# Performance work log

Hardware: AMD Instinct MI355X
Metric: run time of the kernel (lower is better)

## Reference

```python
import jax, jax.numpy as jnp
import numpy as np

NEG_SLOPE = 0.2  # PyG GATConv LeakyReLU slope
EPS = 1e-16


def _add_self_loops(edge_index, num_nodes):
    loops = jnp.arange(num_nodes, dtype=edge_index.dtype)
    return jnp.concatenate([edge_index, jnp.stack([loops, loops])], axis=1)


def _gat_conv(x, src, dst, W, a_src, a_dst, bias, heads, out_ch, concat, num_nodes):
    # x: [N, F_in]; W: [F_in, heads*out_ch]
    h = (x @ W).reshape(num_nodes, heads, out_ch)            # [N, H, C]
    alpha_s = jnp.einsum('nhc,hc->nh', h, a_src)              # [N, H]
    alpha_d = jnp.einsum('nhc,hc->nh', h, a_dst)              # [N, H]
    e = jax.nn.leaky_relu(alpha_s[src] + alpha_d[dst], NEG_SLOPE)  # [E, H]
    # segment softmax over incoming edges of each destination node
    e_max = jax.ops.segment_max(e, dst, num_segments=num_nodes)
    e = jnp.exp(e - e_max[dst])
    denom = jax.ops.segment_sum(e, dst, num_segments=num_nodes)
    alpha = e / (denom[dst] + EPS)                             # [E, H]
    msg = h[src] * alpha[:, :, None]                           # [E, H, C]
    out = jax.ops.segment_sum(msg, dst, num_segments=num_nodes)  # [N, H, C]
    out = out.reshape(num_nodes, heads * out_ch) if concat else out.mean(axis=1)
    return out + bias


def setup_inputs() -> dict:
    key = jax.random.key(0)
    ks = jax.random.split(key, 10)
    N, F_in, H, C1, classes, E = 50000, 128, 8, 16, 40, 1600000
    return {
        'x': jax.random.normal(ks[0], (N, F_in), jnp.float32),
        'edge_index': jax.random.randint(ks[1], (2, E), 0, N, jnp.int64),
        'W1': jax.random.normal(ks[2], (F_in, H * C1), jnp.float32) * (1.0 / np.sqrt(F_in)),
        'a_src1': jax.random.normal(ks[3], (H, C1), jnp.float32) * 0.1,
        'a_dst1': jax.random.normal(ks[4], (H, C1), jnp.float32) * 0.1,
        'b1': jax.random.normal(ks[5], (H * C1,), jnp.float32) * 0.01,
        'W2': jax.random.normal(ks[6], (H * C1, classes), jnp.float32) * (1.0 / np.sqrt(H * C1)),
        'a_src2': jax.random.normal(ks[7], (1, classes), jnp.float32) * 0.1,
        'a_dst2': jax.random.normal(ks[8], (1, classes), jnp.float32) * 0.1,
        'b2': jax.random.normal(ks[9], (classes,), jnp.float32) * 0.01,
    }


def reference(x, edge_index, W1, a_src1, a_dst1, b1, W2, a_src2, a_dst2, b2):
    N = x.shape[0]
    ei = _add_self_loops(edge_index, N)
    src, dst = ei[0], ei[1]
    h = _gat_conv(x, src, dst, W1, a_src1, a_dst1, b1, heads=8, out_ch=16, concat=True, num_nodes=N)
    h = jax.nn.elu(h)
    out = _gat_conv(h, src, dst, W2, a_src2, a_dst2, b2, heads=1, out_ch=40, concat=False, num_nodes=N)
    return out
```

## Files before the change

### kernel.cpp

```cpp
#include <hip/hip_runtime.h>
#include <hip/hip_bf16.h>
#include <hip/hip_fp16.h>

#define NEG_SLOPE 0.2f
#define EPSV 1e-16f
#define CAP 96
#define CHUNK 4096
#define BCAP 9216

static __device__ __forceinline__ float lrelu(float v) {
    return v > 0.0f ? v : NEG_SLOPE * v;
}
static __device__ __forceinline__ float eluf(float v) {
    return v > 0.0f ? v : (__expf(v) - 1.0f);
}

__global__ __launch_bounds__(256) void k_fused1(
    const float* __restrict__ x, const float* __restrict__ W,
    const float* __restrict__ a_src, const float* __restrict__ a_dst,
    const int* __restrict__ ei, int E, int N, int AB,
    __half* __restrict__ h, float* __restrict__ as, float* __restrict__ ad,
    int* __restrict__ gcur, unsigned* __restrict__ bbuf) {
    __shared__ float wl[64 * 128];
    __shared__ float xl[32 * 64];
    const int tid = threadIdx.x;

    if ((int)blockIdx.x < AB) {
        int* cnt = (int*)wl;
        int* base = ((int*)wl) + 256;
        int e0 = blockIdx.x * CHUNK;
        int dreg[16], sreg[16];
#pragma unroll
        for (int jj = 0; jj < 16; ++jj) {
            int e = e0 + tid + jj * 256;
            dreg[jj] = (e < E) ? ei[E + e] : -1;
            sreg[jj] = (e < E) ? ei[e] : 0;
        }
        cnt[tid] = 0;
        __syncthreads();
#pragma unroll
        for (int jj = 0; jj < 16; ++jj)
            if (dreg[jj] >= 0) atomicAdd(&cnt[dreg[jj] >> 8], 1);
        __syncthreads();
        {
            int c = cnt[tid];
            base[tid] = c ? atomicAdd(&gcur[tid], c) : 0;
            cnt[tid] = 0;
        }
        __syncthreads();
#pragma unroll
        for (int jj = 0; jj < 16; ++jj) {
            int d = dreg[jj];
            if (d >= 0) {
                int b = d >> 8;
                int k = atomicAdd(&cnt[b], 1);
                bbuf[(size_t)b * BCAP + base[b] + k] =
                    (unsigned)sreg[jj] | ((unsigned)(d & 255) << 16);
            }
        }
        return;
    }

    const int row0 = (blockIdx.x - AB) * 32;
    const int c0 = (tid & 31) * 4;
    const int r0 = (tid >> 5) * 4;
    float acc[4][4];
#pragma unroll
    for (int r = 0; r < 4; ++r)
#pragma unroll
        for (int c = 0; c < 4; ++c) acc[r][c] = 0.0f;

    for (int kt = 0; kt < 128; kt += 64) {
        __syncthreads();
#pragma unroll
        for (int i = tid * 4; i < 64 * 128; i += 1024)
            *(float4*)&wl[i] = *(const float4*)&W[kt * 128 + i];
#pragma unroll
        for (int i = tid * 4; i < 32 * 64; i += 1024) {
            int r = i >> 6, c = i & 63;
            int gr = row0 + r;
            float4 v = make_float4(0.f, 0.f, 0.f, 0.f);
            if (gr < N) v = *(const float4*)&x[(size_t)gr * 128 + kt + c];
            *(float4*)&xl[i] = v;
        }
        __syncthreads();
#pragma unroll 8
        for (int k = 0; k < 64; ++k) {
            float4 w4 = *(const float4*)&wl[k * 128 + c0];
#pragma unroll
            for (int r = 0; r < 4; ++r) {
                float xv = xl[(r0 + r) * 64 + k];
                acc[r][0] = fmaf(xv, w4.x, acc[r][0]);
                acc[r][1] = fmaf(xv, w4.y, acc[r][1]);
                acc[r][2] = fmaf(xv, w4.z, acc[r][2]);
                acc[r][3] = fmaf(xv, w4.w, acc[r][3]);
            }
        }
    }
#pragma unroll
    for (int r = 0; r < 4; ++r) {
        int gr = row0 + r0 + r;
        if (gr < N) {
            __half2 q0 = __floats2half2_rn(acc[r][0], acc[r][1]);
            __half2 q1 = __floats2half2_rn(acc[r][2], acc[r][3]);
            uint2 st;
            st.x = *(unsigned*)&q0;
            st.y = *(unsigned*)&q1;
            *(uint2*)&h[(size_t)gr * 128 + c0] = st;
        }
    }
    float4 asv = *(const float4*)&a_src[c0];
    float4 adv = *(const float4*)&a_dst[c0];
#pragma unroll
    for (int r = 0; r < 4; ++r) {
        float sp = acc[r][0] * asv.x + acc[r][1] * asv.y + acc[r][2] * asv.z +
                   acc[r][3] * asv.w;
        float dp = acc[r][0] * adv.x + acc[r][1] * adv.y + acc[r][2] * adv.z +
                   acc[r][3] * adv.w;
        sp += __shfl_xor(sp, 1, 64);
        sp += __shfl_xor(sp, 2, 64);
        dp += __shfl_xor(dp, 1, 64);
        dp += __shfl_xor(dp, 2, 64);
        int gr = row0 + r0 + r;
        if ((tid & 3) == 0 && gr < N) {
            int hd = (tid & 31) >> 2;
            as[(size_t)gr * 8 + hd] = sp;
            ad[(size_t)gr * 8 + hd] = dp;
        }
    }
}

__global__ __launch_bounds__(256) void k_csr2(const unsigned* __restrict__ bbuf,
                                              const int* __restrict__ gcnt, int N,
                                              int* __restrict__ deg,
                                              unsigned short* __restrict__ srcs) {
    __shared__ unsigned short rows[256 * CAP];
    __shared__ int cnt[256];
    const int b = blockIdx.x, tid = threadIdx.x;
    cnt[tid] = 0;
    __syncthreads();
    int nb = gcnt[b];
    const unsigned* bp = &bbuf[(size_t)b * BCAP];
    for (int i = tid; i < nb; i += 256) {
        unsigned u = bp[i];
        int dlo = u >> 16;
        int k = atomicAdd(&cnt[dlo], 1);
        rows[dlo * CAP + k] = (unsigned short)(u & 0xFFFFu);
    }
    __syncthreads();
    int n = (b << 8) + tid;
    if (n < N) deg[n] = cnt[tid];
    int maxn = N - (b << 8);
    if (maxn > 256) maxn = 256;
    if (maxn < 0) maxn = 0;
    const unsigned* r32 = (const unsigned*)rows;
    unsigned* g32 = (unsigned*)srcs;
    size_t gbase = (size_t)(b << 8) * (CAP / 2);
    int lim = maxn * (CAP / 2);
    for (int i = tid; i < lim; i += 256) g32[gbase + i] = r32[i];
}

__global__ __launch_bounds__(256) void k_agg1(const int* __restrict__ deg,
                                              const unsigned short* __restrict__ srcs,
                                              const float* __restrict__ as1,
                                              const float* __restrict__ ad1,
                                              const __half* __restrict__ h1,
                                              const float* __restrict__ b1,
                                              __half* __restrict__ hout, int N) {
    int wid = threadIdx.x >> 6, lane = threadIdx.x & 63;
    int n = blockIdx.x * 4 + wid;
    if (n >= N) return;
    size_t st = (size_t)n * CAP;
    int tot = deg[n] + 1;
    int q = lane >> 4;
    int j = lane & 15;
    int es = lane >> 3;
    int hq = lane & 7;
    float adv = ad1[(size_t)n * 8 + hq];
    float l = 0.f;
    float acc[8];
#pragma unroll
    for (int k = 0; k < 8; ++k) acc[k] = 0.f;

    for (int base = 0; base < tot; base += 64) {
        int rem = tot - base;
        if (rem > 64) rem = 64;
        int gi = base + lane;
        int sreg = (gi < tot - 1) ? (int)srcs[st + gi] : n;
        for (int bb = 0; bb < rem; bb += 8) {
            int sp = __shfl(sreg, bb + es, 64);
            float pv = __expf(lrelu(as1[(size_t)sp * 8 + hq] + adv));
            if (bb + es >= rem) pv = 0.f;
            l += pv;
#pragma unroll
            for (int t = 0; t < 8; t += 4) {
                int er = t + q;
                int s = __shfl(sreg, bb + er, 64);
                float p = __shfl(pv, (er << 3) | (j >> 1), 64);
                uint4 u = *(const uint4*)&h1[(size_t)s * 128 + (j << 3)];
                const __half2* hp2 = (const __half2*)&u;
#pragma unroll
                for (int k2 = 0; k2 < 4; ++k2) {
                    float2 f = __half22float2(hp2[k2]);
                    acc[2 * k2]     = fmaf(p, f.x, acc[2 * k2]);
                    acc[2 * k2 + 1] = fmaf(p, f.y, acc[2 * k2 + 1]);
                }
            }
        }
    }
#pragma unroll
    for (int k = 0; k < 8; ++k) {
        acc[k] += __shfl_xor(acc[k], 16, 64);
        acc[k] += __shfl_xor(acc[k], 32, 64);
    }
    l += __shfl_xor(l, 8, 64);
    l += __shfl_xor(l, 16, 64);
    l += __shfl_xor(l, 32, 64);
    float myl = __shfl(l, j >> 1, 64);
    if (q == 0) {
        float rl = 1.f / (myl + EPSV);
        float4 bb0 = *(const float4*)&b1[j * 8];
        float4 bb1 = *(const float4*)&b1[j * 8 + 4];
        float o[8];
        o[0] = eluf(fmaf(acc[0], rl, bb0.x));
        o[1] = eluf(fmaf(acc[1], rl, bb0.y));
        o[2] = eluf(fmaf(acc[2], rl, bb0.z));
        o[3] = eluf(fmaf(acc[3], rl, bb0.w));
        o[4] = eluf(fmaf(acc[4], rl, bb1.x));
        o[5] = eluf(fmaf(acc[5], rl, bb1.y));
        o[6] = eluf(fmaf(acc[6], rl, bb1.z));
        o[7] = eluf(fmaf(acc[7], rl, bb1.w));
        __half2 q0 = __floats2half2_rn(o[0], o[1]);
        __half2 q1 = __floats2half2_rn(o[2], o[3]);
        __half2 q2 = __floats2half2_rn(o[4], o[5]);
        __half2 q3 = __floats2half2_rn(o[6], o[7]);
        uint4 stv;
        stv.x = *(unsigned*)&q0;
        stv.y = *(unsigned*)&q1;
        stv.z = *(unsigned*)&q2;
        stv.w = *(unsigned*)&q3;
        *(uint4*)&hout[(size_t)n * 128 + j * 8] = stv;
    }
}

__global__ __launch_bounds__(256) void k_gemm2(const __half* __restrict__ hin,
                                               const float* __restrict__ W2,
                                               const float* __restrict__ a2s,
                                               const float* __restrict__ a2d,
                                               __half* __restrict__ h2,
                                               float* __restrict__ as2,
                                               float* __restrict__ ad2, int N) {
    __shared__ float wl[128 * 40];
    __shared__ float xl[16 * 128];
    const int tid = threadIdx.x;
    const int n0 = blockIdx.x * 16;
#pragma unroll
    for (int i = tid * 4; i < 128 * 40; i += 1024)
        *(float4*)&wl[i] = *(const float4*)&W2[i];
    {
        int i = tid * 8;
        int r = i >> 7;
        int gr = n0 + r;
        float4 v0 = make_float4(0.f, 0.f, 0.f, 0.f);
        float4 v1 = v0;
        if (gr < N) {
            uint4 u = *(const uint4*)&hin[(size_t)gr * 128 + (i & 127)];
            float2 f0 = __half22float2(*(const __half2*)&u.x);
            float2 f1 = __half22float2(*(const __half2*)&u.y);
            float2 f2 = __half22float2(*(const __half2*)&u.z);
            float2 f3 = __half22float2(*(const __half2*)&u.w);
            v0 = make_float4(f0.x, f0.y, f1.x, f1.y);
            v1 = make_float4(f2.x, f2.y, f3.x, f3.y);
        }
        *(float4*)&xl[i] = v0;
        *(float4*)&xl[i + 4] = v1;
    }
    __syncthreads();
    const int w = tid >> 6, c = tid & 63;
    const int r0 = w * 4;
    float a0 = 0.f, a1 = 0.f, a2 = 0.f, a3 = 0.f;
    if (c < 40) {
        const float* x0 = &xl[(r0 + 0) * 128];
        const float* x1 = &xl[(r0 + 1) * 128];
        const float* x2 = &xl[(r0 + 2) * 128];
        const float* x3 = &xl[(r0 + 3) * 128];
#pragma unroll 8
        for (int k = 0; k < 128; k += 4) {
            float4 q0 = *(const float4*)&x0[k];
            float4 q1 = *(const float4*)&x1[k];
            float4 q2 = *(const float4*)&x2[k];
            float4 q3 = *(const float4*)&x3[k];
            float w0 = wl[(k + 0) * 40 + c];
            float w1 = wl[(k + 1) * 40 + c];
            float w2v = wl[(k + 2) * 40 + c];
            float w3 = wl[(k + 3) * 40 + c];
            a0 = fmaf(q0.x, w0, a0); a0 = fmaf(q0.y, w1, a0);
            a0 = fmaf(q0.z, w2v, a0); a0 = fmaf(q0.w, w3, a0);
            a1 = fmaf(q1.x, w0, a1); a1 = fmaf(q1.y, w1, a1);
            a1 = fmaf(q1.z, w2v, a1); a1 = fmaf(q1.w, w3, a1);
            a2 = fmaf(q2.x, w0, a2); a2 = fmaf(q2.y, w1, a2);
            a2 = fmaf(q2.z, w2v, a2); a2 = fmaf(q2.w, w3, a2);
            a3 = fmaf(q3.x, w0, a3); a3 = fmaf(q3.y, w1, a3);
            a3 = fmaf(q3.z, w2v, a3); a3 = fmaf(q3.w, w3, a3);
        }
    }
    float s2v = (c < 40) ? a2s[c] : 0.f;
    float d2v = (c < 40) ? a2d[c] : 0.f;
    float sv0 = a0 * s2v, dv0 = a0 * d2v;
    float sv1 = a1 * s2v, dv1 = a1 * d2v;
    float sv2 = a2 * s2v, dv2 = a2 * d2v;
    float sv3 = a3 * s2v, dv3 = a3 * d2v;
#pragma unroll
    for (int o = 32; o > 0; o >>= 1) {
        sv0 += __shfl_down(sv0, o, 64);
        dv0 += __shfl_down(dv0, o, 64);
        sv1 += __shfl_down(sv1, o, 64);
        dv1 += __shfl_down(dv1, o, 64);
        sv2 += __shfl_down(sv2, o, 64);
        dv2 += __shfl_down(dv2, o, 64);
        sv3 += __shfl_down(sv3, o, 64);
        dv3 += __shfl_down(dv3, o, 64);
    }
    int g0 = n0 + r0, g1 = g0 + 1, g2 = g0 + 2, g3 = g0 + 3;
    if (c < 40) {
        if (g0 < N) h2[(size_t)g0 * 40 + c] = __float2half(a0);
        if (g1 < N) h2[(size_t)g1 * 40 + c] = __float2half(a1);
        if (g2 < N) h2[(size_t)g2 * 40 + c] = __float2half(a2);
        if (g3 < N) h2[(size_t)g3 * 40 + c] = __float2half(a3);
    }
    if (c == 0) {
        if (g0 < N) { as2[g0] = sv0; ad2[g0] = dv0; }
        if (g1 < N) { as2[g1] = sv1; ad2[g1] = dv1; }
        if (g2 < N) { as2[g2] = sv2; ad2[g2] = dv2; }
        if (g3 < N) { as2[g3] = sv3; ad2[g3] = dv3; }
    }
}

__global__ __launch_bounds__(256) void k_agg2(const int* __restrict__ deg,
                                              const unsigned short* __restrict__ srcs,
                                              const float* __restrict__ as2,
                                              const float* __restrict__ ad2,
                                              const __half* __restrict__ h2,
                                              const float* __restrict__ b2,
                                              float* __restrict__ out, int N) {
    int wid = threadIdx.x >> 6, lane = threadIdx.x & 63;
    int n = blockIdx.x * 4 + wid;
    if (n >= N) return;
    size_t st = (size_t)n * CAP;
    int tot = deg[n] + 1;
    int half = lane >> 5;
    int cl = lane & 31;
    int c0 = cl * 2;
    float adv = ad2[n];
    float l = 0.f;
    float2 acc = make_float2(0.f, 0.f);

    for (int base = 0; base < tot; base += 64) {
        int rem = tot - base;
        if (rem > 64) rem = 64;
        int gi = base + lane;
        int sreg = (gi < tot - 1) ? (int)srcs[st + gi] : n;
        float pv = 0.f;
        if (gi < tot) pv = __expf(lrelu(as2[sreg] + adv));
        l += pv;
        for (int t = 0; t < rem; t += 8) {
            int s_[4];
            float p_[4];
#pragma unroll
            for (int pr = 0; pr < 4; ++pr) {
                int myi = t + 2 * pr + half;
                int ii = myi & 63;
                s_[pr] = __shfl(sreg, ii, 64);
                float pp = __shfl(pv, ii, 64);
                if (myi >= 64) pp = 0.f;
                p_[pr] = pp;
            }
            if (cl < 20) {
#pragma unroll
                for (int pr = 0; pr < 4; ++pr) {
                    float2 hv =
                        __half22float2(*(const __half2*)&h2[(size_t)s_[pr] * 40 + c0]);
                    acc.x = fmaf(p_[pr], hv.x, acc.x);
                    acc.y = fmaf(p_[pr], hv.y, acc.y);
                }
            }
        }
    }
#pragma unroll
    for (int off = 1; off < 64; off <<= 1) l += __shfl_xor(l, off, 64);
    acc.x += __shfl_xor(acc.x, 32, 64);
    acc.y += __shfl_xor(acc.y, 32, 64);
    if (half == 0 && cl < 20) {
        float rl = 1.f / (l + EPSV);
        out[(size_t)n * 40 + c0]     = fmaf(acc.x, rl, b2[c0]);
        out[(size_t)n * 40 + c0 + 1] = fmaf(acc.y, rl, b2[c0 + 1]);
    }
}

extern "C" void kernel_launch(void* const* d_in, const int* in_sizes, int n_in,
                              void* d_out, int out_size, void* d_ws, size_t ws_size,
                              hipStream_t stream) {
    const float* x      = (const float*)d_in[0];
    const int*   ei     = (const int*)d_in[1];
    const float* W1     = (const float*)d_in[2];
    const float* a_src1 = (const float*)d_in[3];
    const float* a_dst1 = (const float*)d_in[4];
    const float* b1     = (const float*)d_in[5];
    const float* W2     = (const float*)d_in[6];
    const float* a_src2 = (const float*)d_in[7];
    const float* a_dst2 = (const float*)d_in[8];
    const float* b2     = (const float*)d_in[9];
    float* out = (float*)d_out;

    const int N = in_sizes[0] / 128;
    const int E = in_sizes[1] / 2;
    const int AB = (E + CHUNK - 1) / CHUNK;
    const int GB = (N + 31) / 32;
    const int NBUCK = (N + 255) >> 8;

    float* ws = (float*)d_ws;
    size_t off = 0;
    auto alloc = [&](size_t nElem) {
        float* p = ws + off;
        off += (nElem + 3) & ~(size_t)3;
        return p;
    };
    __half* h1           = (__half*)alloc((size_t)N * 64);
    __half* hin2         = (__half*)alloc((size_t)N * 64);
    float* as1           = alloc((size_t)N * 8);
    float* ad1           = alloc((size_t)N * 8);
    __half* h2           = (__half*)alloc((size_t)N * 20);
    float* as2           = alloc(N);
    float* ad2           = alloc(N);
    int* deg             = (int*)alloc(N);
    int* gcur            = (int*)alloc(256);
    unsigned short* srcs = (unsigned short*)alloc(((size_t)N * CAP + 1) / 2);
    unsigned* bbuf       = (unsigned*)alloc((size_t)NBUCK * BCAP);

    hipMemsetAsync(gcur, 0, 256 * sizeof(int), stream);

    dim3 B(256);
    k_fused1<<<dim3(AB + GB), B, 0, stream>>>(x, W1, a_src1, a_dst1, ei, E, N, AB,
                                              h1, as1, ad1, gcur, bbuf);
    k_csr2<<<dim3(NBUCK), B, 0, stream>>>(bbuf, gcur, N, deg, srcs);
    k_agg1<<<dim3((N + 3) / 4), B, 0, stream>>>(deg, srcs, as1, ad1, h1, b1, hin2, N);
    k_gemm2<<<dim3((N + 15) / 16), B, 0, stream>>>(hin2, W2, a_src2, a_dst2, h2, as2, ad2, N);
    k_agg2<<<dim3((N + 3) / 4), B, 0, stream>>>(deg, srcs, as2, ad2, h2, b2, out, N);
}
```

Before: 183.5 us.

## Split layer-1 aggregation into four column slices with sliced h1 layout

Stores h1 as four 32-column slices, each contiguous over nodes, and runs the layer-1 aggregation as four launches, one per slice (two heads each). Each slice is 3.2 MB of fp16, small enough to stay in L2/MALL during the random source gathers, which is meant to cut DRAM traffic from gathering. The cost is recomputing the attention exps for each slice, reading deg/srcs four times, extra launches, and 64-byte gathers in place of 256-byte ones.

```diff
diff --git a/kernel.cpp b/kernel.cpp
--- a/kernel.cpp
+++ b/kernel.cpp
@@ -106,7 +106,7 @@
             uint2 st;
             st.x = *(unsigned*)&q0;
             st.y = *(unsigned*)&q1;
-            *(uint2*)&h[(size_t)gr * 128 + c0] = st;
+            *(uint2*)&h[((size_t)(c0 >> 5) * N + gr) * 32 + (c0 & 31)] = st;
         }
     }
     float4 asv = *(const float4*)&a_src[c0];
@@ -160,23 +160,26 @@
     for (int i = tid; i < lim; i += 256) g32[gbase + i] = r32[i];
 }
 
-__global__ __launch_bounds__(256) void k_agg1(const int* __restrict__ deg,
-                                              const unsigned short* __restrict__ srcs,
-                                              const float* __restrict__ as1,
-                                              const float* __restrict__ ad1,
-                                              const __half* __restrict__ h1,
-                                              const float* __restrict__ b1,
-                                              __half* __restrict__ hout, int N) {
+__global__ __launch_bounds__(256) void k_agg1s(const int* __restrict__ deg,
+                                               const unsigned short* __restrict__ srcs,
+                                               const float* __restrict__ as1,
+                                               const float* __restrict__ ad1,
+                                               const __half* __restrict__ h1s,
+                                               const float* __restrict__ b1,
+                                               __half* __restrict__ hout, int N,
+                                               int slice) {
     int wid = threadIdx.x >> 6, lane = threadIdx.x & 63;
     int n = blockIdx.x * 4 + wid;
     if (n >= N) return;
     size_t st = (size_t)n * CAP;
     int tot = deg[n] + 1;
-    int q = lane >> 4;
-    int j = lane & 15;
-    int es = lane >> 3;
-    int hq = lane & 7;
-    float adv = ad1[(size_t)n * 8 + hq];
+    int g = lane >> 2;
+    int j = lane & 3;
+    int es = lane >> 1;
+    int hp = lane & 1;
+    int hh = j >> 1;
+    float adv = ad1[(size_t)n * 8 + slice * 2 + hp];
+    const __half* hs = h1s + (size_t)slice * N * 32;
     float l = 0.f;
     float acc[8];
 #pragma unroll
@@ -187,17 +190,18 @@
         if (rem > 64) rem = 64;
         int gi = base + lane;
         int sreg = (gi < tot - 1) ? (int)srcs[st + gi] : n;
-        for (int bb = 0; bb < rem; bb += 8) {
-            int sp = __shfl(sreg, bb + es, 64);
-            float pv = __expf(lrelu(as1[(size_t)sp * 8 + hq] + adv));
-            if (bb + es >= rem) pv = 0.f;
+        for (int hb = 0; hb < rem; hb += 32) {
+            int sp = __shfl(sreg, hb + es, 64);
+            float pv = __expf(lrelu(as1[(size_t)sp * 8 + slice * 2 + hp] + adv));
+            if (hb + es >= rem) pv = 0.f;
             l += pv;
-#pragma unroll
-            for (int t = 0; t < 8; t += 4) {
-                int er = t + q;
-                int s = __shfl(sreg, bb + er, 64);
-                float p = __shfl(pv, (er << 3) | (j >> 1), 64);
-                uint4 u = *(const uint4*)&h1[(size_t)s * 128 + (j << 3)];
+            int lim = rem - hb;
+            if (lim > 32) lim = 32;
+            for (int t = 0; t < lim; t += 16) {
+                int er = t + g;
+                int s = __shfl(sreg, hb + er, 64);
+                float p = __shfl(pv, (er << 1) | hh, 64);
+                uint4 u = *(const uint4*)&hs[(size_t)s * 32 + (j << 3)];
                 const __half2* hp2 = (const __half2*)&u;
 #pragma unroll
                 for (int k2 = 0; k2 < 4; ++k2) {
@@ -210,17 +214,22 @@
     }
 #pragma unroll
     for (int k = 0; k < 8; ++k) {
+        acc[k] += __shfl_xor(acc[k], 4, 64);
+        acc[k] += __shfl_xor(acc[k], 8, 64);
         acc[k] += __shfl_xor(acc[k], 16, 64);
         acc[k] += __shfl_xor(acc[k], 32, 64);
     }
+    l += __shfl_xor(l, 2, 64);
+    l += __shfl_xor(l, 4, 64);
     l += __shfl_xor(l, 8, 64);
     l += __shfl_xor(l, 16, 64);
     l += __shfl_xor(l, 32, 64);
-    float myl = __shfl(l, j >> 1, 64);
-    if (q == 0) {
-        float rl = 1.f / (myl + EPSV);
-        float4 bb0 = *(const float4*)&b1[j * 8];
-        float4 bb1 = *(const float4*)&b1[j * 8 + 4];
+    float lh = __shfl(l, hh, 64);
+    if (g == 0) {
+        float rl = 1.f / (lh + EPSV);
+        int cb = slice * 32 + (j << 3);
+        float4 bb0 = *(const float4*)&b1[cb];
+        float4 bb1 = *(const float4*)&b1[cb + 4];
         float o[8];
         o[0] = eluf(fmaf(acc[0], rl, bb0.x));
         o[1] = eluf(fmaf(acc[1], rl, bb0.y));
@@ -239,7 +248,7 @@
         stv.y = *(unsigned*)&q1;
         stv.z = *(unsigned*)&q2;
         stv.w = *(unsigned*)&q3;
-        *(uint4*)&hout[(size_t)n * 128 + j * 8] = stv;
+        *(uint4*)&hout[(size_t)n * 128 + cb] = stv;
     }
 }
 
@@ -443,7 +452,9 @@
     k_fused1<<<dim3(AB + GB), B, 0, stream>>>(x, W1, a_src1, a_dst1, ei, E, N, AB,
                                               h1, as1, ad1, gcur, bbuf);
     k_csr2<<<dim3(NBUCK), B, 0, stream>>>(bbuf, gcur, N, deg, srcs);
-    k_agg1<<<dim3((N + 3) / 4), B, 0, stream>>>(deg, srcs, as1, ad1, h1, b1, hin2, N);
+    for (int s = 0; s < 4; ++s)
+        k_agg1s<<<dim3((N + 3) / 4), B, 0, stream>>>(deg, srcs, as1, ad1, h1, b1,
+                                                     hin2, N, s);
     k_gemm2<<<dim3((N + 15) / 16), B, 0, stream>>>(hin2, W2, a_src2, a_dst2, h2, as2, ad2, N);
     k_agg2<<<dim3((N + 3) / 4), B, 0, stream>>>(deg, srcs, as2, ad2, h2, b2, out, N);
 }
```

Result: slower. 255.4 us (+39.2%).
